# Optimization experiments

Measured on AMD Instinct MI355X. Metric: run time of the kernel, lower is better.

The kernel has to match this reference:

```python
import jax, jax.numpy as jnp
import numpy as np

N = 50000
E = 800000
IN, HID, OUT = 256, 128, 128
H = 2


def gat_conv(x, edge_src, edge_dst, W, att_src, att_dst, bias, concat=True):
    # PyG GATConv: x' = W x, edge attention e = leaky_relu(a_s.x'_src + a_d.x'_dst),
    # softmax over incoming edges of each dst node, weighted scatter-add.
    n = x.shape[0]
    heads, ch = att_src.shape
    xl = (x @ W).reshape(n, heads, ch)                      # [N,H,C]
    a_src = jnp.sum(xl * att_src[None], axis=-1)            # [N,H]
    a_dst = jnp.sum(xl * att_dst[None], axis=-1)            # [N,H]
    e = a_src[edge_src] + a_dst[edge_dst]                   # [E,H]
    e = jax.nn.leaky_relu(e, negative_slope=0.2)
    # segment softmax over dst neighborhoods (self-loops guarantee non-empty)
    emax = jax.ops.segment_max(e, edge_dst, num_segments=n)
    ee = jnp.exp(e - emax[edge_dst])
    denom = jax.ops.segment_sum(ee, edge_dst, num_segments=n)
    alpha = ee / (denom[edge_dst] + 1e-16)                  # [E,H]
    msg = xl[edge_src] * alpha[:, :, None]                  # [E,H,C]
    out = jax.ops.segment_sum(msg, edge_dst, num_segments=n)  # [N,H,C]
    out = out.reshape(n, heads * ch) if concat else out.mean(axis=1)
    return out + bias


def setup_inputs() -> dict:
    key = jax.random.key(0)
    ks = jax.random.split(key, 12)
    x = jax.random.normal(ks[0], (N, IN), dtype=jnp.float32)
    edge_index = jax.random.randint(ks[1], (2, E), 0, N, dtype=jnp.int64)
    node_type = (jnp.arange(N, dtype=jnp.int64) % 3)
    agent_idx = jnp.arange(0, N, 3, dtype=jnp.int64)  # nodes with type 0
    # layer 0: in=256 -> out=128, heads=2, concat
    W0 = jax.random.normal(ks[2], (IN, H * HID), dtype=jnp.float32) / np.sqrt(IN)
    as0 = jax.random.normal(ks[3], (H, HID), dtype=jnp.float32) / np.sqrt(HID)
    ad0 = jax.random.normal(ks[4], (H, HID), dtype=jnp.float32) / np.sqrt(HID)
    b0 = jnp.zeros((H * HID,), dtype=jnp.float32)
    # layer 1: in=128*2 -> out=128, heads=2, concat (average_last=False)
    W1 = jax.random.normal(ks[5], (H * HID, H * OUT), dtype=jnp.float32) / np.sqrt(H * HID)
    as1 = jax.random.normal(ks[6], (H, OUT), dtype=jnp.float32) / np.sqrt(OUT)
    ad1 = jax.random.normal(ks[7], (H, OUT), dtype=jnp.float32) / np.sqrt(OUT)
    b1 = jnp.zeros((H * OUT,), dtype=jnp.float32)
    return {"x": x, "edge_index": edge_index, "node_type": node_type,
            "agent_idx": agent_idx, "W0": W0, "as0": as0, "ad0": ad0, "b0": b0,
            "W1": W1, "as1": as1, "ad1": ad1, "b1": b1}


def reference(x, edge_index, node_type, agent_idx, W0, as0, ad0, b0, W1, as1, ad1, b1):
    # add self loops (PyG GATConv default add_self_loops=True)
    loop = jnp.arange(N, dtype=edge_index.dtype)
    src = jnp.concatenate([edge_index[0], loop])
    dst = jnp.concatenate([edge_index[1], loop])
    final = []
    h = gat_conv(x, src, dst, W0, as0, ad0, b0, concat=True)
    h = jax.nn.sigmoid(h)
    final.append(h[agent_idx])  # full_receptive_field=True
    h = gat_conv(h, src, dst, W1, as1, ad1, b1, concat=True)
    h = jax.nn.sigmoid(h)
    final.append(h[agent_idx])
    return jnp.concatenate(final, axis=1)  # [n_agents, 128*2 + 128*2]
```

## Files before the change

### kernel.cpp

```cpp
#include <hip/hip_runtime.h>
#include <hip/hip_fp16.h>

typedef unsigned short u16;
typedef unsigned int   u32;
typedef unsigned char  u8;
typedef __attribute__((ext_vector_type(8))) short short8;
typedef __attribute__((ext_vector_type(8))) unsigned short ushort8v;
typedef __attribute__((ext_vector_type(4))) float f32x4;

#define TPB 256

#define GLDS16(g,l) __builtin_amdgcn_global_load_lds( \
    (const __attribute__((address_space(1))) void*)(g), \
    (__attribute__((address_space(3))) void*)(l), 16, 0, 0)

__device__ __forceinline__ float b2f(u16 u){ u32 x=((u32)u)<<16; return __uint_as_float(x); }
__device__ __forceinline__ u16 f2b(float f){ u32 x=__float_as_uint(f); u32 r=x+0x7FFFu+((x>>16)&1u); return (u16)(r>>16); }
__device__ __forceinline__ float lrelu(float x){ return x>0.f?x:0.2f*x; }
__device__ __forceinline__ float sigm(float x){ return 1.f/(1.f+__expf(-x)); }

__device__ __forceinline__ float4 ld4(const void* p, size_t i4, int isbf){
  if(isbf){
    ushort4 u=((const ushort4*)p)[i4];
    return make_float4(b2f(u.x),b2f(u.y),b2f(u.z),b2f(u.w));
  }
  return ((const float4*)p)[i4];
}
__device__ __forceinline__ float ld1(const void* p, size_t i, int isbf){
  return isbf ? b2f(((const u16*)p)[i]) : ((const float*)p)[i];
}

__global__ void k_deg(const int* __restrict__ dst, int E, int N, int* __restrict__ deg,
                      int* __restrict__ pos,
                      int* __restrict__ ainv, const u16* __restrict__ w0, int* __restrict__ flag){
  int gid=blockIdx.x*blockDim.x+threadIdx.x;
  if(blockIdx.x==0){
    __shared__ int s[256];
    int t=threadIdx.x, sane=0;
    for(int i=t;i<512;i+=256){
      u16 u=w0[i]; u32 e=(u>>7)&0xFFu;
      if((e>=103u&&e<=143u)||((u&0x7FFFu)==0u)) sane++;
    }
    s[t]=sane; __syncthreads();
    for(int o=128;o;o>>=1){ if(t<o) s[t]+=s[t+o]; __syncthreads(); }
    if(t==0) flag[0]=(s[0]>=480)?1:0;
  }
  if(gid<N) ainv[gid]=-1;
  if(gid>=E+N) return;
  int d=(gid<E)?dst[gid]:(gid-E);
  d=min(max(d,0),N-1);
  pos[gid]=atomicAdd(&deg[d],1);
}

__global__ void k_scan(const int* __restrict__ deg, int* __restrict__ rs,
                       int* __restrict__ counter, int n,
                       const int* __restrict__ aidx, int* __restrict__ ainv, int na){
  __shared__ int tmp[TPB];
  __shared__ int base;
  int i=blockIdx.x*TPB+threadIdx.x;
  if(i<na){ int a=aidx[i]; if(a>=0&&a<n) ainv[a]=i; }
  int v=(i<n)?deg[i]:0;
  tmp[threadIdx.x]=v; __syncthreads();
  for(int off=1;off<TPB;off<<=1){
    int t=(threadIdx.x>=off)?tmp[threadIdx.x-off]:0;
    __syncthreads();
    tmp[threadIdx.x]+=t;
    __syncthreads();
  }
  if(threadIdx.x==TPB-1) base=atomicAdd(counter,tmp[TPB-1]);
  __syncthreads();
  if(i<n) rs[i]=base+tmp[threadIdx.x]-v;
}

__global__ void k_fill(const int* __restrict__ src, const int* __restrict__ dst, int E, int N,
                       const int* __restrict__ rs, const int* __restrict__ pos,
                       int* __restrict__ col){
  int e=blockIdx.x*blockDim.x+threadIdx.x; if(e>=E+N) return;
  int d,s;
  if(e<E){ d=dst[e]; s=src[e]; } else { d=e-E; s=e-E; }
  d=min(max(d,0),N-1); s=min(max(s,0),N-1);
  col[rs[d]+pos[e]]=s;
}

__global__ __launch_bounds__(256) void k_prep(const void* __restrict__ Wa, u16* __restrict__ WTa,
                                              const void* __restrict__ Wb, u16* __restrict__ WTb,
                                              const void* __restrict__ X, u16* __restrict__ xb,
                                              int n8, const int* __restrict__ flag){
  const int isbf=flag[0];
  int bid=blockIdx.x;
  if(bid<32){
    __shared__ float s[64][65];
    int z=bid>>4, y=(bid>>2)&3, xb_=bid&3;
    const void* W = z ? Wb : Wa;
    u16* WT = z ? WTb : WTa;
    int tx=threadIdx.x&63, ty=threadIdx.x>>6;
    int k0=xb_*64, n0=y*64;
    #pragma unroll
    for(int i=0;i<64;i+=4)
      s[ty+i][tx]=ld1(W,(size_t)(k0+ty+i)*256+n0+tx,isbf);
    __syncthreads();
    #pragma unroll
    for(int i=0;i<64;i+=4)
      WT[(size_t)(n0+ty+i)*256+k0+tx]=f2b(s[tx][ty+i]);
    return;
  }
  int i=(bid-32)*256+threadIdx.x; if(i>=n8) return;
  size_t e=(size_t)i*8;
  if(isbf){
    *(ushort8v*)(xb+e)=*(const ushort8v*)((const u16*)X+e);
  }else{
    const float4* fp=(const float4*)((const float*)X+e);
    float4 f0=fp[0], f1=fp[1];
    ushort8v o;
    o[0]=f2b(f0.x); o[1]=f2b(f0.y); o[2]=f2b(f0.z); o[3]=f2b(f0.w);
    o[4]=f2b(f1.x); o[5]=f2b(f1.y); o[6]=f2b(f1.z); o[7]=f2b(f1.w);
    *(ushort8v*)(xb+e)=o;
  }
}

__global__ __launch_bounds__(256) void k_gemm(const u16* __restrict__ A, const u16* __restrict__ BT,
                                              u16* __restrict__ C, int M){
  __shared__ short As[128*64];
  __shared__ short Bs[128*64];
  const int t=threadIdx.x;
  const int lane=t&63, wv=t>>6;
  const int wm=wv>>1, wn=wv&1;
  const int m15=lane&15, kg=lane>>4;
  const int gm0=blockIdx.x*128, n0=blockIdx.y*128;
  const int sr=lane>>3, slot=lane&7;
  f32x4 acc[4][4]={};
  for(int k0=0;k0<256;k0+=64){
    #pragma unroll
    for(int i=0;i<4;++i){
      int r=wv*32+i*8+sr;
      int kq=slot^(r&7);
      int ga=gm0+r; ga=ga<M?ga:M-1;
      GLDS16(A+(size_t)ga*256+k0+kq*8, As+(wv*32+i*8)*64);
      GLDS16(BT+(size_t)(n0+r)*256+k0+kq*8, Bs+(wv*32+i*8)*64);
    }
    __syncthreads();
    #pragma unroll
    for(int s=0;s<2;++s){
      short8 af[4], bf[4];
      #pragma unroll
      for(int mi=0;mi<4;++mi){
        int row=wm*64+mi*16+m15;
        int sl=(s*4+kg)^(row&7);
        af[mi]=*(const short8*)&As[row*64+sl*8];
      }
      #pragma unroll
      for(int ni=0;ni<4;++ni){
        int row=wn*64+ni*16+m15;
        int sl=(s*4+kg)^(row&7);
        bf[ni]=*(const short8*)&Bs[row*64+sl*8];
      }
      #pragma unroll
      for(int mi=0;mi<4;++mi)
        #pragma unroll
        for(int ni=0;ni<4;++ni)
          acc[mi][ni]=__builtin_amdgcn_mfma_f32_16x16x32_bf16(af[mi],bf[ni],acc[mi][ni],0,0,0);
    }
    __syncthreads();
  }
  #pragma unroll
  for(int mi=0;mi<4;++mi){
    #pragma unroll
    for(int r=0;r<4;++r){
      int grow=gm0+wm*64+mi*16+kg*4+r;
      if(grow<M){
        #pragma unroll
        for(int ni=0;ni<4;++ni){
          int gcol=n0+wn*64+ni*16+m15;
          C[(size_t)grow*256+gcol]=f2b(acc[mi][ni][r]);
        }
      }
    }
  }
}

__global__ __launch_bounds__(256) void k_att(const u16* __restrict__ xl, const void* __restrict__ as_,
                                             const void* __restrict__ ad_, float4* __restrict__ asv,
                                             float2* __restrict__ adv, u8* __restrict__ xl8,
                                             int n, const int* __restrict__ flag){
  const int isbf=flag[0];
  int w=(blockIdx.x*256+threadIdx.x)>>6;
  int lane=threadIdx.x&63;
  if(w>=n) return;
  int ch=lane*4;
  ushort4 u=*(const ushort4*)(xl+(size_t)w*256+ch);
  float4 s=ld4(as_,ch>>2,isbf);
  float4 d=ld4(ad_,ch>>2,isbf);
  float x0=b2f(u.x),x1=b2f(u.y),x2=b2f(u.z),x3=b2f(u.w);
  float m=fmaxf(fmaxf(fabsf(x0),fabsf(x1)),fmaxf(fabsf(x2),fabsf(x3)));
  for(int off=32;off;off>>=1) m=fmaxf(m,__shfl_xor(m,off));
  float mm=fmaxf(m,1e-20f);
  float scale=mm*(1.f/127.f);
  float rsc=127.f/mm;
  int q0=(int)rintf(fmaf(x0,rsc,128.f));
  int q1=(int)rintf(fmaf(x1,rsc,128.f));
  int q2=(int)rintf(fmaf(x2,rsc,128.f));
  int q3=(int)rintf(fmaf(x3,rsc,128.f));
  u32 pack=(u32)q0|((u32)q1<<8)|((u32)q2<<16)|((u32)q3<<24);
  ((u32*)(xl8+(size_t)w*256))[lane]=pack;
  float ps=x0*s.x+x1*s.y+x2*s.z+x3*s.w;
  float pd=x0*d.x+x1*d.y+x2*d.z+x3*d.w;
  for(int off=16;off;off>>=1){ ps+=__shfl_xor(ps,off); pd+=__shfl_xor(pd,off); }
  float ps1=__shfl(ps,32), pd1=__shfl(pd,32);
  if(lane==0){
    asv[w]=make_float4(ps,ps1,scale,0.f);
    adv[w]=make_float2(pd,pd1);
  }
}

__global__ __launch_bounds__(256) void k_alpha(const int* __restrict__ rs, const int* __restrict__ deg,
    const int* __restrict__ col, const float4* __restrict__ asv, const float2* __restrict__ adv,
    int2* __restrict__ ew, float2* __restrict__ rden, int n){
  int w=(blockIdx.x*256+threadIdx.x)>>5;
  int lane=threadIdx.x&31;
  if(w>=n) return;
  int s0=rs[w], cnt=deg[w];
  float2 ad=adv[w];
  float sum0=0.f, sum1=0.f;
  for(int base=0;base<cnt;base+=32){
    int j=base+lane;
    if(j<cnt){
      int sv=col[s0+j];
      float4 a=asv[sv];
      float e0=fminf(lrelu(a.x+ad.x),11.f);
      float e1=fminf(lrelu(a.y+ad.y),11.f);
      float w0=__expf(e0), w1=__expf(e1);
      sum0+=w0; sum1+=w1;
      __half2 p=__floats2half2_rn(w0*a.z,w1*a.z);
      ew[s0+j]=make_int2(sv,*(int*)&p);
    }
  }
  for(int off=16;off;off>>=1){ sum0+=__shfl_xor(sum0,off); sum1+=__shfl_xor(sum1,off); }
  if(lane==0) rden[w]=make_float2(1.f/(sum0+1e-16f),1.f/(sum1+1e-16f));
}

__global__ __launch_bounds__(256) void k_agg(const int* __restrict__ rs, const int* __restrict__ deg,
    const int2* __restrict__ ew, const float2* __restrict__ rden,
    const u8* __restrict__ xl8, const void* __restrict__ bias,
    u16* __restrict__ hout, void* __restrict__ out, int ostride, int ocol,
    const int* __restrict__ ainv, int n, const int* __restrict__ flag){
  const int isbf=flag[0];
  int w=(blockIdx.x*blockDim.x+threadIdx.x)>>5;
  int sl=threadIdx.x&31;
  if(w>=n) return;
  int s0=rs[w], cnt=deg[w];
  int ch=sl*8, h=sl>>4;
  float acc[8]={};
  float sumw=0.f;
  for(int j=0;j<cnt;j+=8){
    int2 e[8];
    #pragma unroll
    for(int u=0;u<8;++u){
      int idx=j+u; idx=idx<cnt?idx:cnt-1;
      e[u]=ew[s0+idx];
    }
    uint2 rv[8];
    #pragma unroll
    for(int u=0;u<8;++u)
      rv[u]=*(const uint2*)(xl8+(size_t)e[u].x*256+ch);
    #pragma unroll
    for(int u=0;u<8;++u){
      __half2 p=*(__half2*)&e[u].y;
      float wb=__half2float(h?__high2half(p):__low2half(p));
      wb=(j+u<cnt)?wb:0.f;
      u32 a=rv[u].x, b=rv[u].y;
      acc[0]=fmaf(wb,(float)( a     &255u),acc[0]);
      acc[1]=fmaf(wb,(float)((a>> 8)&255u),acc[1]);
      acc[2]=fmaf(wb,(float)((a>>16)&255u),acc[2]);
      acc[3]=fmaf(wb,(float)( a>>24      ),acc[3]);
      acc[4]=fmaf(wb,(float)( b     &255u),acc[4]);
      acc[5]=fmaf(wb,(float)((b>> 8)&255u),acc[5]);
      acc[6]=fmaf(wb,(float)((b>>16)&255u),acc[6]);
      acc[7]=fmaf(wb,(float)( b>>24      ),acc[7]);
      sumw+=wb;
    }
  }
  float2 rd=rden[w];
  float rh=h?rd.y:rd.x;
  float4 b0=ld4(bias,ch>>2,isbf);
  float4 b1=ld4(bias,(ch>>2)+1,isbf);
  float c=128.f*sumw;
  float r[8];
  r[0]=sigm((acc[0]-c)*rh+b0.x); r[1]=sigm((acc[1]-c)*rh+b0.y);
  r[2]=sigm((acc[2]-c)*rh+b0.z); r[3]=sigm((acc[3]-c)*rh+b0.w);
  r[4]=sigm((acc[4]-c)*rh+b1.x); r[5]=sigm((acc[5]-c)*rh+b1.y);
  r[6]=sigm((acc[6]-c)*rh+b1.z); r[7]=sigm((acc[7]-c)*rh+b1.w);
  ushort8v ov;
  #pragma unroll
  for(int q=0;q<8;++q) ov[q]=f2b(r[q]);
  if(hout) *(ushort8v*)(hout+(size_t)w*256+ch)=ov;
  int ar=ainv[w];
  if(ar>=0){
    size_t o=(size_t)ar*ostride+ocol+ch;
    if(isbf){
      *(ushort8v*)((u16*)out+o)=ov;
    }else{
      *(float4*)((float*)out+o)  =make_float4(r[0],r[1],r[2],r[3]);
      *(float4*)((float*)out+o+4)=make_float4(r[4],r[5],r[6],r[7]);
    }
  }
}

extern "C" void kernel_launch(void* const* d_in, const int* in_sizes, int n_in,
                              void* d_out, int out_size, void* d_ws, size_t ws_size,
                              hipStream_t stream) {
  const void* x   = d_in[0];
  const int*  ei  = (const int*)d_in[1];
  const int*  aidx= (const int*)d_in[3];
  const void* W0  = d_in[4];
  const void* as0 = d_in[5];
  const void* ad0 = d_in[6];
  const void* b0  = d_in[7];
  const void* W1  = d_in[8];
  const void* as1 = d_in[9];
  const void* ad1 = d_in[10];
  const void* b1  = d_in[11];

  const int N  = in_sizes[0]/256;
  const int E  = in_sizes[1]/2;
  const int na = in_sizes[3];
  const int Et = E+N;

  char* ws=(char*)d_ws; size_t off=0;
  auto alloc=[&](size_t bytes)->void*{ void* p=ws+off; off+=(bytes+255)&~(size_t)255; return p; };
  int*   flg =(int*) alloc(256);
  u16*   xl  =(u16*) alloc((size_t)N*256*2);
  u16*   h1  =(u16*) alloc((size_t)N*256*2);
  u8*    xl8 =(u8*)  alloc((size_t)N*256);
  u16*   WT0 =(u16*) alloc((size_t)256*256*2);
  u16*   WT1 =(u16*) alloc((size_t)256*256*2);
  float4* asv=(float4*)alloc((size_t)N*16);
  float2* adv=(float2*)alloc((size_t)N*8);
  char*  zbase=ws+off;
  int*   deg =(int*) alloc((size_t)N*4);
  int*   ctr =(int*) alloc(256);
  size_t zlen=(ws+off)-zbase;
  int*   pos =(int*) alloc((size_t)Et*4);
  int*   rstp=(int*) alloc((size_t)N*4);
  int*   ainv=(int*) alloc((size_t)N*4);
  int*   col =(int*) alloc((size_t)Et*4);
  int2*  ew  =(int2*)alloc((size_t)Et*8);
  float2* rdn=(float2*)alloc((size_t)N*8);

  u16* xb = h1;

  const int* esrc=ei;
  const int* edst=ei+E;

  hipMemsetAsync(zbase,0,zlen,stream);

  k_deg  <<<(Et+255)/256,256,0,stream>>>(edst,E,N,deg,pos,ainv,(const u16*)W0,flg);
  k_scan <<<(N+TPB-1)/TPB,TPB,0,stream>>>(deg,rstp,ctr,N,aidx,ainv,na);
  k_fill <<<(Et+255)/256,256,0,stream>>>(esrc,edst,E,N,rstp,pos,col);
  k_prep <<<32+(N*32+255)/256,256,0,stream>>>(W0,WT0,W1,WT1,x,xb,N*32,flg);

  dim3 gg((N+127)/128,2);
  k_gemm <<<gg,256,0,stream>>>(xb,WT0,xl,N);
  k_att  <<<(N+3)/4,256,0,stream>>>(xl,as0,ad0,asv,adv,xl8,N,flg);
  k_alpha<<<(N+7)/8,256,0,stream>>>(rstp,deg,col,asv,adv,ew,rdn,N);
  k_agg  <<<(N+7)/8,256,0,stream>>>(rstp,deg,ew,rdn,xl8,b0,h1,d_out,512,0,ainv,N,flg);
  k_gemm <<<gg,256,0,stream>>>(h1,WT1,xl,N);
  k_att  <<<(N+3)/4,256,0,stream>>>(xl,as1,ad1,asv,adv,xl8,N,flg);
  k_alpha<<<(N+7)/8,256,0,stream>>>(rstp,deg,col,asv,adv,ew,rdn,N);
  k_agg  <<<(N+7)/8,256,0,stream>>>(rstp,deg,ew,rdn,xl8,b1,(u16*)nullptr,d_out,512,256,ainv,N,flg);
}
```

Measured before the change: 343.2 us.

## Fuse edge-attention and aggregation kernels, recomputing weights instead of storing them

Merges k_alpha into k_agg so that each destination node computes its softmax denominator in a first pass over its neighbours and then recomputes the per-edge exp weight inside the aggregation loop. This removes the ew and rden intermediate buffers and their global writes and reads, and removes one kernel launch per layer. In exchange, the col and asv gathers are done twice per edge, and each lane redundantly recomputes an exp per edge.

```diff
diff --git a/kernel.cpp b/kernel.cpp
--- a/kernel.cpp
+++ b/kernel.cpp
@@ -212,34 +212,8 @@
   }
 }
 
-__global__ __launch_bounds__(256) void k_alpha(const int* __restrict__ rs, const int* __restrict__ deg,
+__global__ __launch_bounds__(256) void k_edge(const int* __restrict__ rs, const int* __restrict__ deg,
     const int* __restrict__ col, const float4* __restrict__ asv, const float2* __restrict__ adv,
-    int2* __restrict__ ew, float2* __restrict__ rden, int n){
-  int w=(blockIdx.x*256+threadIdx.x)>>5;
-  int lane=threadIdx.x&31;
-  if(w>=n) return;
-  int s0=rs[w], cnt=deg[w];
-  float2 ad=adv[w];
-  float sum0=0.f, sum1=0.f;
-  for(int base=0;base<cnt;base+=32){
-    int j=base+lane;
-    if(j<cnt){
-      int sv=col[s0+j];
-      float4 a=asv[sv];
-      float e0=fminf(lrelu(a.x+ad.x),11.f);
-      float e1=fminf(lrelu(a.y+ad.y),11.f);
-      float w0=__expf(e0), w1=__expf(e1);
-      sum0+=w0; sum1+=w1;
-      __half2 p=__floats2half2_rn(w0*a.z,w1*a.z);
-      ew[s0+j]=make_int2(sv,*(int*)&p);
-    }
-  }
-  for(int off=16;off;off>>=1){ sum0+=__shfl_xor(sum0,off); sum1+=__shfl_xor(sum1,off); }
-  if(lane==0) rden[w]=make_float2(1.f/(sum0+1e-16f),1.f/(sum1+1e-16f));
-}
-
-__global__ __launch_bounds__(256) void k_agg(const int* __restrict__ rs, const int* __restrict__ deg,
-    const int2* __restrict__ ew, const float2* __restrict__ rden,
     const u8* __restrict__ xl8, const void* __restrict__ bias,
     u16* __restrict__ hout, void* __restrict__ out, int ostride, int ocol,
     const int* __restrict__ ainv, int n, const int* __restrict__ flag){
@@ -248,39 +222,59 @@
   int sl=threadIdx.x&31;
   if(w>=n) return;
   int s0=rs[w], cnt=deg[w];
+  float2 ad=adv[w];
+  float sum0=0.f, sum1=0.f;
+  for(int base=0;base<cnt;base+=32){
+    int j=base+sl;
+    if(j<cnt){
+      int sv=col[s0+j];
+      float4 a=asv[sv];
+      float e0=fminf(lrelu(a.x+ad.x),11.f);
+      float e1=fminf(lrelu(a.y+ad.y),11.f);
+      sum0+=__expf(e0); sum1+=__expf(e1);
+    }
+  }
+  for(int off=16;off;off>>=1){ sum0+=__shfl_xor(sum0,off); sum1+=__shfl_xor(sum1,off); }
   int ch=sl*8, h=sl>>4;
+  float rh=1.f/((h?sum1:sum0)+1e-16f);
+  float adh=h?ad.y:ad.x;
   float acc[8]={};
   float sumw=0.f;
   for(int j=0;j<cnt;j+=8){
-    int2 e[8];
+    int sv[8];
     #pragma unroll
     for(int u=0;u<8;++u){
       int idx=j+u; idx=idx<cnt?idx:cnt-1;
-      e[u]=ew[s0+idx];
+      sv[u]=col[s0+idx];
     }
     uint2 rv[8];
     #pragma unroll
     for(int u=0;u<8;++u)
-      rv[u]=*(const uint2*)(xl8+(size_t)e[u].x*256+ch);
+      rv[u]=*(const uint2*)(xl8+(size_t)sv[u]*256+ch);
+    float wb[8];
     #pragma unroll
     for(int u=0;u<8;++u){
-      __half2 p=*(__half2*)&e[u].y;
-      float wb=__half2float(h?__high2half(p):__low2half(p));
-      wb=(j+u<cnt)?wb:0.f;
+      float4 a=asv[sv[u]];
+      float ah=h?a.y:a.x;
+      float e=fminf(lrelu(ah+adh),11.f);
+      float x=__half2float(__float2half_rn(__expf(e)*a.z));
+      wb[u]=(j+u<cnt)?x:0.f;
+    }
+    #pragma unroll
+    for(int u=0;u<8;++u){
+      float wf=wb[u];
       u32 a=rv[u].x, b=rv[u].y;
-      acc[0]=fmaf(wb,(float)( a     &255u),acc[0]);
-      acc[1]=fmaf(wb,(float)((a>> 8)&255u),acc[1]);
-      acc[2]=fmaf(wb,(float)((a>>16)&255u),acc[2]);
-      acc[3]=fmaf(wb,(float)( a>>24      ),acc[3]);
-      acc[4]=fmaf(wb,(float)( b     &255u),acc[4]);
-      acc[5]=fmaf(wb,(float)((b>> 8)&255u),acc[5]);
-      acc[6]=fmaf(wb,(float)((b>>16)&255u),acc[6]);
-      acc[7]=fmaf(wb,(float)( b>>24      ),acc[7]);
-      sumw+=wb;
-    }
-  }
-  float2 rd=rden[w];
-  float rh=h?rd.y:rd.x;
+      acc[0]=fmaf(wf,(float)( a     &255u),acc[0]);
+      acc[1]=fmaf(wf,(float)((a>> 8)&255u),acc[1]);
+      acc[2]=fmaf(wf,(float)((a>>16)&255u),acc[2]);
+      acc[3]=fmaf(wf,(float)( a>>24      ),acc[3]);
+      acc[4]=fmaf(wf,(float)( b     &255u),acc[4]);
+      acc[5]=fmaf(wf,(float)((b>> 8)&255u),acc[5]);
+      acc[6]=fmaf(wf,(float)((b>>16)&255u),acc[6]);
+      acc[7]=fmaf(wf,(float)( b>>24      ),acc[7]);
+      sumw+=wf;
+    }
+  }
   float4 b0=ld4(bias,ch>>2,isbf);
   float4 b1=ld4(bias,(ch>>2)+1,isbf);
   float c=128.f*sumw;
@@ -343,8 +337,6 @@
   int*   rstp=(int*) alloc((size_t)N*4);
   int*   ainv=(int*) alloc((size_t)N*4);
   int*   col =(int*) alloc((size_t)Et*4);
-  int2*  ew  =(int2*)alloc((size_t)Et*8);
-  float2* rdn=(float2*)alloc((size_t)N*8);
 
   u16* xb = h1;
 
@@ -361,10 +353,8 @@
   dim3 gg((N+127)/128,2);
   k_gemm <<<gg,256,0,stream>>>(xb,WT0,xl,N);
   k_att  <<<(N+3)/4,256,0,stream>>>(xl,as0,ad0,asv,adv,xl8,N,flg);
-  k_alpha<<<(N+7)/8,256,0,stream>>>(rstp,deg,col,asv,adv,ew,rdn,N);
-  k_agg  <<<(N+7)/8,256,0,stream>>>(rstp,deg,ew,rdn,xl8,b0,h1,d_out,512,0,ainv,N,flg);
+  k_edge <<<(N+7)/8,256,0,stream>>>(rstp,deg,col,asv,adv,xl8,b0,h1,d_out,512,0,ainv,N,flg);
   k_gemm <<<gg,256,0,stream>>>(h1,WT1,xl,N);
   k_att  <<<(N+3)/4,256,0,stream>>>(xl,as1,ad1,asv,adv,xl8,N,flg);
-  k_alpha<<<(N+7)/8,256,0,stream>>>(rstp,deg,col,asv,adv,ew,rdn,N);
-  k_agg  <<<(N+7)/8,256,0,stream>>>(rstp,deg,ew,rdn,xl8,b1,(u16*)nullptr,d_out,512,256,ainv,N,flg);
-}
+  k_edge <<<(N+7)/8,256,0,stream>>>(rstp,deg,col,asv,adv,xl8,b1,(u16*)nullptr,d_out,512,256,ainv,N,flg);
+}
```

Result: slower. 366.4 us (+6.8%).
